# Optimization experiments

Measured on AMD Instinct MI355X. Metric: run time of the kernel, lower is better.

Reference implementation:

```python
import jax, jax.numpy as jnp
import numpy as np

D_MODEL = 1024
D_STATE = 64
D_CONV = 4
HEADDIM = 64
EXPAND = 2
NGROUPS = 1
D_INNER = EXPAND * D_MODEL            # 2048
NHEADS = D_INNER // HEADDIM           # 32
CONV_DIM = D_INNER + 2 * NGROUPS * D_STATE
D_IN_PROJ = 2 * D_INNER + 2 * NGROUPS * D_STATE + NHEADS
FFN_DIM = 4096
B_SZ = 2
SEQ = 2048


def layernorm(x, w, b, eps=1e-5):
    m = jnp.mean(x, axis=-1, keepdims=True)
    v = jnp.var(x, axis=-1, keepdims=True)
    return (x - m) * jax.lax.rsqrt(v + eps) * w + b


def silu(x):
    return x * jax.nn.sigmoid(x)


def causal_dwconv(x, w, b):
    # x: [B, L, C], w: [C, K] depthwise, b: [C]; causal (left) padding
    xc = jnp.transpose(x, (0, 2, 1))                       # [B, C, L]
    xc = jnp.pad(xc, ((0, 0), (0, 0), (D_CONV - 1, 0)))
    k = w[:, None, :]                                      # [C, 1, K]
    y = jax.lax.conv_general_dilated(
        xc, k, window_strides=(1,), padding='VALID',
        dimension_numbers=('NCH', 'OIH', 'NCH'),
        feature_group_count=CONV_DIM)
    return jnp.transpose(y, (0, 2, 1)) + b                 # [B, L, C]


def mamba2(x, in_proj_w, conv_w, conv_b, dt_bias, A_log, D_param, norm_w, out_proj_w):
    Bsz, L, _ = x.shape
    zxbcdt = x @ in_proj_w.T                               # [B, L, D_IN_PROJ]
    z, xBC, dt = jnp.split(zxbcdt, [D_INNER, D_INNER + CONV_DIM], axis=-1)
    dt = jax.nn.softplus(dt + dt_bias)                     # [B, L, H]
    xBC = silu(causal_dwconv(xBC, conv_w, conv_b))
    xs, Bm, Cm = jnp.split(xBC, [D_INNER, D_INNER + NGROUPS * D_STATE], axis=-1)
    xs = xs.reshape(Bsz, L, NHEADS, HEADDIM)
    Bm = Bm.reshape(Bsz, L, NGROUPS, D_STATE)
    Cm = Cm.reshape(Bsz, L, NGROUPS, D_STATE)
    hpg = NHEADS // NGROUPS
    Bh = jnp.repeat(Bm, hpg, axis=2)                       # [B, L, H, N]
    Ch = jnp.repeat(Cm, hpg, axis=2)                       # [B, L, H, N]
    A = -jnp.exp(A_log)                                    # [H]
    dA = jnp.exp(dt * A)                                   # [B, L, H]

    # time-major for scan
    def step(h, inp):
        dA_t, dt_t, x_t, B_t, C_t = inp                    # [B,H], [B,H], [B,H,P], [B,H,N], [B,H,N]
        h = h * dA_t[:, :, None, None] + (dt_t[:, :, None, None] * x_t[..., None]) * B_t[:, :, None, :]
        y_t = jnp.einsum('bhpn,bhn->bhp', h, C_t)
        return h, y_t

    h0 = jnp.zeros((Bsz, NHEADS, HEADDIM, D_STATE), dtype=x.dtype)
    xs_tm = (jnp.moveaxis(dA, 1, 0), jnp.moveaxis(dt, 1, 0),
             jnp.moveaxis(xs, 1, 0), jnp.moveaxis(Bh, 1, 0), jnp.moveaxis(Ch, 1, 0))
    _, ys = jax.lax.scan(step, h0, xs_tm)                  # [L, B, H, P]
    y = jnp.moveaxis(ys, 0, 1) + D_param[None, None, :, None] * xs
    y = y.reshape(Bsz, L, D_INNER)
    # gated RMSNorm: RMSNorm(y * silu(z)) * weight
    y = y * silu(z)
    y = y * jax.lax.rsqrt(jnp.mean(jnp.square(y), axis=-1, keepdims=True) + 1e-5) * norm_w
    return y @ out_proj_w.T                                # [B, L, D_MODEL]


def setup_inputs() -> dict:
    key = jax.random.key(0)
    ks = jax.random.split(key, 12)
    s = 0.02
    inp = {
        'x': jax.random.normal(ks[0], (B_SZ, SEQ, D_MODEL), dtype=jnp.float32),
        'ln0_w': jnp.ones((D_MODEL,), jnp.float32), 'ln0_b': jnp.zeros((D_MODEL,), jnp.float32),
        'ln1_w': jnp.ones((D_MODEL,), jnp.float32), 'ln1_b': jnp.zeros((D_MODEL,), jnp.float32),
        'ln2_w': jnp.ones((D_MODEL,), jnp.float32), 'ln2_b': jnp.zeros((D_MODEL,), jnp.float32),
        'in_proj_w': jax.random.normal(ks[1], (D_IN_PROJ, D_MODEL), jnp.float32) * s,
        'conv_w': jax.random.normal(ks[2], (CONV_DIM, D_CONV), jnp.float32) * 0.2,
        'conv_b': jnp.zeros((CONV_DIM,), jnp.float32),
        'dt_bias': jax.random.uniform(ks[3], (NHEADS,), jnp.float32, -4.0, -1.0),
        'A_log': jnp.log(jnp.arange(1, NHEADS + 1, dtype=jnp.float32)),
        'D_param': jnp.ones((NHEADS,), jnp.float32),
        'norm_w': jnp.ones((D_INNER,), jnp.float32),
        'out_proj_w': jax.random.normal(ks[4], (D_MODEL, D_INNER), jnp.float32) * s,
        'ffn_w1': jax.random.normal(ks[5], (FFN_DIM, D_MODEL), jnp.float32) * s,
        'ffn_b1': jnp.zeros((FFN_DIM,), jnp.float32),
        'ffn_w2': jax.random.normal(ks[6], (D_MODEL, FFN_DIM), jnp.float32) * s,
        'ffn_b2': jnp.zeros((D_MODEL,), jnp.float32),
    }
    return inp


def reference(x, ln0_w, ln0_b, ln1_w, ln1_b, ln2_w, ln2_b, in_proj_w, conv_w, conv_b,
              dt_bias, A_log, D_param, norm_w, out_proj_w, ffn_w1, ffn_b1, ffn_w2, ffn_b2):
    x = layernorm(x, ln0_w, ln0_b)                                  # ln0 (layer_id==0)
    m = mamba2(layernorm(x, ln1_w, ln1_b), in_proj_w, conv_w, conv_b,
               dt_bias, A_log, D_param, norm_w, out_proj_w)
    x = x + m                                                        # dropout is identity in eval
    h = layernorm(x, ln2_w, ln2_b)
    h = jax.nn.gelu(h @ ffn_w1.T + ffn_b1, approximate=False) @ ffn_w2.T + ffn_b2
    return x + h
```

## Files before the change

kernel.cpp:

```cpp
#include <hip/hip_runtime.h>
#include <hip/hip_bf16.h>
#include <math.h>

typedef __hip_bfloat16 bf16;
typedef __bf16 bhalf;
typedef bhalf bhalf8 __attribute__((ext_vector_type(8)));
typedef float f32x4 __attribute__((ext_vector_type(4)));
typedef unsigned short u16;
typedef u16 u16x4 __attribute__((ext_vector_type(4)));
typedef u16 u16x8 __attribute__((ext_vector_type(8)));

#define D_MODEL   1024
#define D_STATE   64
#define HEADDIM   64
#define D_INNER   2048
#define NHEADS    32
#define CONV_DIM  2176
#define D_IN_PROJ 4256
#define FFN_DIM   4096
#define BSZ       2
#define SEQ       2048
#define NROWS     (BSZ*SEQ)
#define TC        64
#define NCH       (SEQ/TC)

#define AS1 __attribute__((address_space(1)))
#define AS3 __attribute__((address_space(3)))
__device__ __forceinline__ void load_lds16(const void* g, void* l) {
  __builtin_amdgcn_global_load_lds((AS1 void*)g, (AS3 void*)l, 16, 0, 0);
}

__device__ __forceinline__ float bf2f(u16 u) {
  return __uint_as_float(((unsigned)u) << 16);
}
__device__ __forceinline__ u16 f2bbits(float f) {
  bf16 h = __float2bfloat16(f);
  return *(u16*)&h;
}

#define NT 18
struct CvtArgs {
  const void* src[NT];
  void*       dst[NT];
  int ccum[NT + 1];
  int nel[NT];
};

__global__ __launch_bounds__(256)
void cvt_kernel(CvtArgs a, const unsigned short* __restrict__ x0,
                int* __restrict__ flagp)
{
  __shared__ int sbad;
  if (threadIdx.x == 0) sbad = 0;
  __syncthreads();
  {
    float v = bf2f(x0[threadIdx.x]);
    if (!(fabsf(v) <= 1e6f)) sbad = 1;
  }
  __syncthreads();
  const int isf32 = sbad;
  if (blockIdx.x == 0 && threadIdx.x == 0) *flagp = isf32;

  int c = blockIdx.x;
  int ti = 0;
  while (c >= a.ccum[ti + 1]) ti++;
  int j = (c - a.ccum[ti]) * 2048 + threadIdx.x * 8;
  if (j >= a.nel[ti]) return;
  if (isf32) {
    const float* s = (const float*)a.src[ti];
    f32x4 v0 = *(const f32x4*)(s + j);
    f32x4 v1 = *(const f32x4*)(s + j + 4);
    u16x8 o;
    #pragma unroll
    for (int k = 0; k < 4; k++) { o[k] = f2bbits(v0[k]); o[k + 4] = f2bbits(v1[k]); }
    *(u16x8*)((u16*)a.dst[ti] + j) = o;
  } else {
    *(u16x8*)((u16*)a.dst[ti] + j) = *(const u16x8*)((const u16*)a.src[ti] + j);
  }
}

template<int EPI>
__global__ __launch_bounds__(256, 2)
void gemm_bt(const bf16* __restrict__ A, const bf16* __restrict__ W,
             int M, int N, int K,
             bf16* __restrict__ outB,
             const bf16* __restrict__ bias)
{
  __shared__ __align__(16) bhalf sA[2][128 * 64];
  __shared__ __align__(16) bhalf sW[2][128 * 64];
  const int n0   = blockIdx.x * 128;
  const int m0   = blockIdx.y * 128;
  const int t    = threadIdx.x;
  const int w    = t >> 6;
  const int lane = t & 63;
  const int wm   = (w >> 1) * 64;
  const int wn   = (w & 1) * 64;
  const int lr   = lane & 15;
  const int lq   = lane >> 4;

  f32x4 acc[4][4];
  #pragma unroll
  for (int i = 0; i < 4; i++)
    #pragma unroll
    for (int j = 0; j < 4; j++)
      acc[i][j] = (f32x4){0.f, 0.f, 0.f, 0.f};

  auto stage = [&](int buf, int kk0) {
    #pragma unroll
    for (int j = 0; j < 4; j++) {
      int s  = t + 256 * j;
      int r  = s >> 3;
      int cs = (s & 7) ^ (r & 7);
      load_lds16(A + (size_t)(m0 + r) * K + kk0 + cs * 8, &sA[buf][s * 8]);
      int wr = n0 + r; wr = wr < N ? wr : N - 1;
      load_lds16(W + (size_t)wr * K + kk0 + cs * 8, &sW[buf][s * 8]);
    }
  };

  stage(0, 0);
  __syncthreads();

  int cur = 0;
  for (int k0 = 0; k0 < K; k0 += 64) {
    if (k0 + 64 < K) stage(cur ^ 1, k0 + 64);
    const bhalf* pA = sA[cur];
    const bhalf* pW = sW[cur];
    #pragma unroll
    for (int kk = 0; kk < 2; kk++) {
      bhalf8 af[4], bfr[4];
      #pragma unroll
      for (int i = 0; i < 4; i++) {
        int r = wm + i * 16 + lr;
        int c = (kk * 4 + lq) ^ (r & 7);
        af[i] = *(const bhalf8*)(pA + r * 64 + c * 8);
      }
      #pragma unroll
      for (int j = 0; j < 4; j++) {
        int r = wn + j * 16 + lr;
        int c = (kk * 4 + lq) ^ (r & 7);
        bfr[j] = *(const bhalf8*)(pW + r * 64 + c * 8);
      }
      #pragma unroll
      for (int i = 0; i < 4; i++)
        #pragma unroll
        for (int j = 0; j < 4; j++)
          acc[i][j] = __builtin_amdgcn_mfma_f32_16x16x32_bf16(af[i], bfr[j], acc[i][j], 0, 0, 0);
    }
    __syncthreads();
    cur ^= 1;
  }

  #pragma unroll
  for (int i = 0; i < 4; i++) {
    #pragma unroll
    for (int j = 0; j < 4; j++) {
      #pragma unroll
      for (int r = 0; r < 4; r++) {
        int m = m0 + wm + i * 16 + lq * 4 + r;
        int n = n0 + wn + j * 16 + lr;
        if (n < N) {
          float v = acc[i][j][r];
          size_t idx = (size_t)m * N + n;
          if (EPI == 0) {
            outB[idx] = __float2bfloat16(v);
          } else {
            v += __bfloat162float(bias[n]);
            outB[idx] = __float2bfloat16(0.5f * v * (1.0f + erff(v * 0.70710678118654752f)));
          }
        }
      }
    }
  }
}

struct SkParts4 { float* p[4]; };

template<int SK>
__global__ __launch_bounds__(256, 4)
void gemm_skinny_sk(const bf16* __restrict__ A, const bf16* __restrict__ W,
                    int M, int N, int K, SkParts4 parts)
{
  __shared__ __align__(16) bhalf sA[64 * 64];
  __shared__ __align__(16) bhalf sW[128 * 64];
  const int id   = blockIdx.x;
  const int z    = id >> 9;
  const int id9  = id & 511;
  const int hi   = id9 >> 6;
  const int rem  = id9 & 63;
  const int jn   = rem >> 3;
  const int mi   = hi * 8 + (rem & 7);
  const int m0   = mi * 64;
  const int n0   = jn * 128;
  const int t    = threadIdx.x;
  const int w    = t >> 6;
  const int lane = t & 63;
  const int wm   = (w >> 1) * 32;
  const int wn   = (w & 1) * 64;
  const int lr   = lane & 15;
  const int lq   = lane >> 4;

  f32x4 acc[2][4];
  #pragma unroll
  for (int i = 0; i < 2; i++)
    #pragma unroll
    for (int j = 0; j < 4; j++)
      acc[i][j] = (f32x4){0.f, 0.f, 0.f, 0.f};

  const int kh = K / SK;
  const int kend = z * kh + kh;
  for (int k0 = z * kh; k0 < kend; k0 += 64) {
    #pragma unroll
    for (int j = 0; j < 2; j++) {
      int s  = t + 256 * j;
      int r  = s >> 3;
      int cs = (s & 7) ^ (r & 7);
      load_lds16(A + (size_t)(m0 + r) * K + k0 + cs * 8, sA + s * 8);
    }
    #pragma unroll
    for (int j = 0; j < 4; j++) {
      int s  = t + 256 * j;
      int r  = s >> 3;
      int cs = (s & 7) ^ (r & 7);
      load_lds16(W + (size_t)(n0 + r) * K + k0 + cs * 8, sW + s * 8);
    }
    __syncthreads();
    #pragma unroll
    for (int kk = 0; kk < 2; kk++) {
      bhalf8 af[2], bfr[4];
      #pragma unroll
      for (int i = 0; i < 2; i++) {
        int r = wm + i * 16 + lr;
        int c = (kk * 4 + lq) ^ (r & 7);
        af[i] = *(const bhalf8*)(sA + r * 64 + c * 8);
      }
      #pragma unroll
      for (int j = 0; j < 4; j++) {
        int r = wn + j * 16 + lr;
        int c = (kk * 4 + lq) ^ (r & 7);
        bfr[j] = *(const bhalf8*)(sW + r * 64 + c * 8);
      }
      #pragma unroll
      for (int i = 0; i < 2; i++)
        #pragma unroll
        for (int j = 0; j < 4; j++)
          acc[i][j] = __builtin_amdgcn_mfma_f32_16x16x32_bf16(af[i], bfr[j], acc[i][j], 0, 0, 0);
    }
    __syncthreads();
  }

  float* out = parts.p[z];
  #pragma unroll
  for (int i = 0; i < 2; i++)
    #pragma unroll
    for (int j = 0; j < 4; j++)
      #pragma unroll
      for (int r = 0; r < 4; r++) {
        int m = m0 + wm + i * 16 + lq * 4 + r;
        int n = n0 + wn + j * 16 + lr;
        out[(size_t)m * N + n] = acc[i][j][r];
      }
}

__global__ __launch_bounds__(256)
void reduce_out_ln2_kernel(const float* __restrict__ p0, const float* __restrict__ p1,
                           const bf16* __restrict__ resB, float* __restrict__ x2f,
                           const bf16* __restrict__ w, const bf16* __restrict__ b,
                           bf16* __restrict__ hln)
{
  int row = blockIdx.x, t = threadIdx.x;
  int i = row * 256 + t;
  __shared__ float rs[4], rq[4];
  f32x4 a = ((const f32x4*)p0)[i];
  f32x4 bb = ((const f32x4*)p1)[i];
  u16x4 r = ((const u16x4*)resB)[i];
  f32x4 o;
  float s = 0.f, ss = 0.f;
  #pragma unroll
  for (int j = 0; j < 4; j++) {
    o[j] = a[j] + bb[j] + bf2f(r[j]);
    s += o[j]; ss += o[j] * o[j];
  }
  ((f32x4*)x2f)[i] = o;
  #pragma unroll
  for (int off = 32; off; off >>= 1) { s += __shfl_down(s, off); ss += __shfl_down(ss, off); }
  if ((t & 63) == 0) { rs[t >> 6] = s; rq[t >> 6] = ss; }
  __syncthreads();
  float S = rs[0] + rs[1] + rs[2] + rs[3];
  float Q = rq[0] + rq[1] + rq[2] + rq[3];
  float mean = S * (1.f / D_MODEL);
  float rstd = rsqrtf(Q * (1.f / D_MODEL) - mean * mean + 1e-5f);
  u16x4 wv = ((const u16x4*)w)[t];
  u16x4 bv = ((const u16x4*)b)[t];
  u16x4 ov;
  #pragma unroll
  for (int j = 0; j < 4; j++)
    ov[j] = f2bbits((o[j] - mean) * rstd * bf2f(wv[j]) + bf2f(bv[j]));
  ((u16x4*)hln)[i] = ov;
}

__global__ __launch_bounds__(256)
void reduce_ffn_kernel(const float* __restrict__ p0, const float* __restrict__ p1,
                       const float* __restrict__ p2, const float* __restrict__ p3,
                       const bf16* __restrict__ bias, const float* __restrict__ resF,
                       void* __restrict__ outp, const int* __restrict__ flagp)
{
  int i = blockIdx.x * 256 + threadIdx.x;
  int n4 = i & (D_MODEL / 4 - 1);
  f32x4 v0 = ((const f32x4*)p0)[i];
  f32x4 v1 = ((const f32x4*)p1)[i];
  f32x4 v2 = ((const f32x4*)p2)[i];
  f32x4 v3 = ((const f32x4*)p3)[i];
  f32x4 rf = ((const f32x4*)resF)[i];
  u16x4 bb = ((const u16x4*)bias)[n4];
  f32x4 o;
  #pragma unroll
  for (int j = 0; j < 4; j++)
    o[j] = ((v0[j] + v1[j]) + (v2[j] + v3[j])) + rf[j] + bf2f(bb[j]);
  if (*flagp) {
    ((f32x4*)outp)[i] = o;
  } else {
    u16x4 ov;
    #pragma unroll
    for (int j = 0; j < 4; j++) ov[j] = f2bbits(o[j]);
    ((u16x4*)outp)[i] = ov;
  }
}

__global__ __launch_bounds__(256)
void ln01_kernel(const void* __restrict__ xin, const int* __restrict__ flagp,
                 const bf16* __restrict__ w0, const bf16* __restrict__ b0,
                 const bf16* __restrict__ w1, const bf16* __restrict__ b1,
                 bf16* __restrict__ x0o, bf16* __restrict__ x1o)
{
  int row = blockIdx.x, t = threadIdx.x;
  int i = row * 256 + t;
  __shared__ float rs[4], rq[4];
  float v[4], s = 0.f, ss = 0.f;
  if (*flagp) {
    f32x4 xv = ((const f32x4*)xin)[i];
    #pragma unroll
    for (int j = 0; j < 4; j++) v[j] = xv[j];
  } else {
    u16x4 xv = ((const u16x4*)xin)[i];
    #pragma unroll
    for (int j = 0; j < 4; j++) v[j] = bf2f(xv[j]);
  }
  #pragma unroll
  for (int j = 0; j < 4; j++) { s += v[j]; ss += v[j] * v[j]; }
  #pragma unroll
  for (int o = 32; o; o >>= 1) { s += __shfl_down(s, o); ss += __shfl_down(ss, o); }
  if ((t & 63) == 0) { rs[t >> 6] = s; rq[t >> 6] = ss; }
  __syncthreads();
  float S = rs[0] + rs[1] + rs[2] + rs[3];
  float Q = rq[0] + rq[1] + rq[2] + rq[3];
  float mean = S * (1.f / D_MODEL);
  float rstd = rsqrtf(Q * (1.f / D_MODEL) - mean * mean + 1e-5f);
  u16x4 w0v = ((const u16x4*)w0)[t], b0v = ((const u16x4*)b0)[t];
  float u[4]; s = 0.f; ss = 0.f;
  u16x4 o0;
  #pragma unroll
  for (int j = 0; j < 4; j++) {
    u[j] = (v[j] - mean) * rstd * bf2f(w0v[j]) + bf2f(b0v[j]);
    s += u[j]; ss += u[j] * u[j];
    o0[j] = f2bbits(u[j]);
  }
  ((u16x4*)x0o)[i] = o0;
  __syncthreads();
  #pragma unroll
  for (int o = 32; o; o >>= 1) { s += __shfl_down(s, o); ss += __shfl_down(ss, o); }
  if ((t & 63) == 0) { rs[t >> 6] = s; rq[t >> 6] = ss; }
  __syncthreads();
  S = rs[0] + rs[1] + rs[2] + rs[3];
  Q = rq[0] + rq[1] + rq[2] + rq[3];
  mean = S * (1.f / D_MODEL);
  rstd = rsqrtf(Q * (1.f / D_MODEL) - mean * mean + 1e-5f);
  u16x4 w1v = ((const u16x4*)w1)[t], b1v = ((const u16x4*)b1)[t];
  u16x4 o1;
  #pragma unroll
  for (int j = 0; j < 4; j++)
    o1[j] = f2bbits((u[j] - mean) * rstd * bf2f(w1v[j]) + bf2f(b1v[j]));
  ((u16x4*)x1o)[i] = o1;
}

__device__ __forceinline__ void conv8(const bf16* __restrict__ zxb,
                                      const bf16* __restrict__ cw,
                                      const bf16* __restrict__ cb,
                                      bf16* __restrict__ xact, int row, int c0)
{
  int l = row & (SEQ - 1);
  float acc[8];
  {
    bhalf8 cbv = *(const bhalf8*)(cb + c0);
    #pragma unroll
    for (int j = 0; j < 8; j++) acc[j] = (float)cbv[j];
  }
  bhalf wts[32];
  #pragma unroll
  for (int q = 0; q < 4; q++)
    *(bhalf8*)(wts + q * 8) = *(const bhalf8*)(cw + c0 * 4 + q * 8);
  #pragma unroll
  for (int k = 0; k < 4; k++) {
    int lt = l - 3 + k;
    if (lt >= 0) {
      bhalf8 xv = *(const bhalf8*)(zxb + (size_t)(row - 3 + k) * D_IN_PROJ + D_INNER + c0);
      #pragma unroll
      for (int j = 0; j < 8; j++)
        acc[j] = fmaf((float)xv[j], (float)wts[j * 4 + k], acc[j]);
    }
  }
  bhalf8 o;
  #pragma unroll
  for (int j = 0; j < 8; j++) {
    float a = acc[j];
    o[j] = (bhalf)(a / (1.f + expf(-a)));
  }
  *(bhalf8*)(xact + (size_t)row * CONV_DIM + c0) = o;
}

__global__ __launch_bounds__(256)
void conv_silu_dt_kernel(const bf16* __restrict__ zxb, const bf16* __restrict__ cw,
                         const bf16* __restrict__ cb, bf16* __restrict__ xact,
                         const bf16* __restrict__ dtb, const bf16* __restrict__ alog,
                         float* __restrict__ dts, float* __restrict__ ldab)
{
  const int row = blockIdx.y;
  const int t = threadIdx.x;
  if (blockIdx.x == 0) {
    conv8(zxb, cw, cb, xact, row, t * 8);
  } else {
    if (t < 16) {
      conv8(zxb, cw, cb, xact, row, 2048 + t * 8);
    } else if (t < 48) {
      int h = t - 16;
      float v = __bfloat162float(zxb[(size_t)row * D_IN_PROJ + (D_INNER + CONV_DIM) + h]) +
                __bfloat162float(dtb[h]);
      float sp = (v > 20.f) ? v : log1pf(expf(v));
      dts[row * NHEADS + h] = sp;
      ldab[row * NHEADS + h] = -sp * expf(__bfloat162float(alog[h]));
    }
  }
}

__global__ __launch_bounds__(256)
void scan_state_kernel(const bf16* __restrict__ xact, const float* __restrict__ dts,
                       const float* __restrict__ ldab, bf16* __restrict__ Sbuf,
                       float* __restrict__ acb)
{
  __shared__ __align__(16) bf16 wBT[64][72];
  __shared__ __align__(16) bf16 XT[64][72];
  __shared__ float lsS[64], dtS[64];
  const int bid = blockIdx.x;
  const int bh = bid & 63, c = bid >> 6;
  const int b = bh >> 5, h = bh & 31;
  const int t0 = c * TC;
  const int tid = threadIdx.x;
  const int w = tid >> 6, lane = tid & 63;
  const int lr = lane & 15, lq = lane >> 4;

  if (w == 0) {
    float v = ldab[(size_t)(b * SEQ + t0 + lane) * NHEADS + h];
    #pragma unroll
    for (int o = 1; o < 64; o <<= 1) {
      float up = __shfl_up(v, o);
      if (lane >= o) v += up;
    }
    lsS[lane] = v;
    dtS[lane] = dts[(size_t)(b * SEQ + t0 + lane) * NHEADS + h];
  }
  __syncthreads();
  const float lsT = lsS[63];
  {
    int nn = tid & 63, u0 = (tid >> 6) * 16;
    for (int i = 0; i < 16; i++) {
      int u = u0 + i;
      const bf16* rowp = xact + (size_t)(b * SEQ + t0 + u) * CONV_DIM;
      float wgt = dtS[u] * __expf(lsT - lsS[u]);
      wBT[nn][u] = __float2bfloat16(__bfloat162float(rowp[D_INNER + nn]) * wgt);
      XT[nn][u]  = rowp[h * 64 + nn];
    }
  }
  __syncthreads();

  bhalf8 af0 = *(const bhalf8*)&wBT[16 * w + lr][lq * 8];
  bhalf8 af1 = *(const bhalf8*)&wBT[16 * w + lr][32 + lq * 8];
  bf16* sb = Sbuf + ((size_t)bh * NCH + c) * 4096;
  #pragma unroll
  for (int jt = 0; jt < 4; jt++) {
    bhalf8 xf0 = *(const bhalf8*)&XT[16 * jt + lr][lq * 8];
    bhalf8 xf1 = *(const bhalf8*)&XT[16 * jt + lr][32 + lq * 8];
    f32x4 acc = (f32x4){0.f, 0.f, 0.f, 0.f};
    acc = __builtin_amdgcn_mfma_f32_16x16x32_bf16(af0, xf0, acc, 0, 0, 0);
    acc = __builtin_amdgcn_mfma_f32_16x16x32_bf16(af1, xf1, acc, 0, 0, 0);
    #pragma unroll
    for (int r = 0; r < 4; r++) {
      int n = 16 * w + lq * 4 + r;
      int p = 16 * jt + lr;
      sb[p * 64 + n] = __float2bfloat16(acc[r]);
    }
  }
  if (tid == 0) acb[bh * NCH + c] = __expf(lsT);
}

__global__ __launch_bounds__(256)
void state_prop_kernel(bf16* __restrict__ Sbuf, const float* __restrict__ acb)
{
  const int bh = blockIdx.x >> 2, q = blockIdx.x & 3;
  const int t = threadIdx.x;
  bf16* sp = Sbuf + (size_t)bh * NCH * 4096 + q * 1024 + t;
  const float* ap = acb + bh * NCH;
  float h0 = 0.f, h1 = 0.f, h2 = 0.f, h3 = 0.f;
  for (int c = 0; c < NCH; c++) {
    bf16* pc = sp + (size_t)c * 4096;
    float s0 = __bfloat162float(pc[0]);
    float s1 = __bfloat162float(pc[256]);
    float s2 = __bfloat162float(pc[512]);
    float s3 = __bfloat162float(pc[768]);
    float a = ap[c];
    pc[0]   = __float2bfloat16(h0);
    pc[256] = __float2bfloat16(h1);
    pc[512] = __float2bfloat16(h2);
    pc[768] = __float2bfloat16(h3);
    h0 = fmaf(h0, a, s0); h1 = fmaf(h1, a, s1);
    h2 = fmaf(h2, a, s2); h3 = fmaf(h3, a, s3);
  }
}

__global__ __launch_bounds__(256)
void scan_y_kernel(const bf16* __restrict__ xact, const float* __restrict__ dts,
                   const float* __restrict__ ldab, const bf16* __restrict__ Sbuf,
                   bf16* __restrict__ yfull)
{
  __shared__ __align__(16) bf16 Cs[64][72];
  __shared__ __align__(16) bf16 Bs[64][72];
  __shared__ __align__(16) bf16 XT[64][72];
  __shared__ __align__(16) bf16 HT[64][72];
  __shared__ float lsS[64], dtS[64];
  const int bid = blockIdx.x;
  const int bh = bid & 63, c = bid >> 6;
  const int b = bh >> 5, h = bh & 31;
  const int t0 = c * TC;
  const int tid = threadIdx.x;
  const int w = tid >> 6, lane = tid & 63;
  const int lr = lane & 15, lq = lane >> 4;

  if (w == 0) {
    float v = ldab[(size_t)(b * SEQ + t0 + lane) * NHEADS + h];
    #pragma unroll
    for (int o = 1; o < 64; o <<= 1) {
      float up = __shfl_up(v, o);
      if (lane >= o) v += up;
    }
    lsS[lane] = v;
    dtS[lane] = dts[(size_t)(b * SEQ + t0 + lane) * NHEADS + h];
  }
  {
    int nn = tid & 63, u0 = (tid >> 6) * 16;
    for (int i = 0; i < 16; i++) {
      int u = u0 + i;
      const bf16* rowp = xact + (size_t)(b * SEQ + t0 + u) * CONV_DIM;
      Bs[u][nn] = rowp[D_INNER + nn];
      Cs[u][nn] = rowp[D_INNER + 64 + nn];
      XT[nn][u] = rowp[h * 64 + nn];
    }
    const bf16* sb = Sbuf + ((size_t)bh * NCH + c) * 4096;
    for (int i = 0; i < 16; i++) {
      int e = tid + 256 * i;
      HT[e >> 6][e & 63] = sb[e];
    }
  }
  __syncthreads();

  bhalf8 cf0 = *(const bhalf8*)&Cs[16 * w + lr][lq * 8];
  bhalf8 cf1 = *(const bhalf8*)&Cs[16 * w + lr][32 + lq * 8];
  f32x4 accH[4];
  float mreg[4][4];
  #pragma unroll
  for (int jt = 0; jt < 4; jt++) {
    bhalf8 bf0 = *(const bhalf8*)&Bs[16 * jt + lr][lq * 8];
    bhalf8 bf1 = *(const bhalf8*)&Bs[16 * jt + lr][32 + lq * 8];
    f32x4 g = (f32x4){0.f, 0.f, 0.f, 0.f};
    g = __builtin_amdgcn_mfma_f32_16x16x32_bf16(cf0, bf0, g, 0, 0, 0);
    g = __builtin_amdgcn_mfma_f32_16x16x32_bf16(cf1, bf1, g, 0, 0, 0);
    bhalf8 hf0 = *(const bhalf8*)&HT[16 * jt + lr][lq * 8];
    bhalf8 hf1 = *(const bhalf8*)&HT[16 * jt + lr][32 + lq * 8];
    f32x4 ah = (f32x4){0.f, 0.f, 0.f, 0.f};
    ah = __builtin_amdgcn_mfma_f32_16x16x32_bf16(cf0, hf0, ah, 0, 0, 0);
    ah = __builtin_amdgcn_mfma_f32_16x16x32_bf16(cf1, hf1, ah, 0, 0, 0);
    accH[jt] = ah;
    #pragma unroll
    for (int r = 0; r < 4; r++) {
      int t = 16 * w + lq * 4 + r;
      int u = 16 * jt + lr;
      float m = 0.f;
      if (u <= t) m = g[r] * __expf(lsS[t] - lsS[u]) * dtS[u];
      mreg[jt][r] = m;
    }
  }
  __syncthreads();
  #pragma unroll
  for (int jt = 0; jt < 4; jt++)
    #pragma unroll
    for (int r = 0; r < 4; r++)
      Bs[16 * w + lq * 4 + r][16 * jt + lr] = __float2bfloat16(mreg[jt][r]);
  __syncthreads();

  bhalf8 mf0 = *(const bhalf8*)&Bs[16 * w + lr][lq * 8];
  bhalf8 mf1 = *(const bhalf8*)&Bs[16 * w + lr][32 + lq * 8];
  #pragma unroll
  for (int jt = 0; jt < 4; jt++) {
    bhalf8 xf0 = *(const bhalf8*)&XT[16 * jt + lr][lq * 8];
    bhalf8 xf1 = *(const bhalf8*)&XT[16 * jt + lr][32 + lq * 8];
    f32x4 acc = (f32x4){0.f, 0.f, 0.f, 0.f};
    acc = __builtin_amdgcn_mfma_f32_16x16x32_bf16(mf0, xf0, acc, 0, 0, 0);
    acc = __builtin_amdgcn_mfma_f32_16x16x32_bf16(mf1, xf1, acc, 0, 0, 0);
    #pragma unroll
    for (int r = 0; r < 4; r++) {
      int t = 16 * w + lq * 4 + r;
      int p = 16 * jt + lr;
      float y = acc[r] + __expf(lsS[t]) * accH[jt][r];
      yfull[(size_t)(b * SEQ + t0 + t) * D_INNER + h * 64 + p] = __float2bfloat16(y);
    }
  }
}

__global__ __launch_bounds__(256)
void gate_rms_kernel(const bf16* __restrict__ yfull, const bf16* __restrict__ xact,
                     const bf16* __restrict__ zxb, const bf16* __restrict__ Dp,
                     const bf16* __restrict__ nw, bf16* __restrict__ yn)
{
  int row = blockIdx.x, t = threadIdx.x;
  int c0 = t * 8;
  __shared__ float rq[4];
  bhalf8 yv8 = *(const bhalf8*)(yfull + (size_t)row * D_INNER + c0);
  bhalf8 xv8 = *(const bhalf8*)(xact + (size_t)row * CONV_DIM + c0);
  bhalf8 zv8 = *(const bhalf8*)(zxb + (size_t)row * D_IN_PROJ + c0);
  float Dv = __bfloat162float(Dp[c0 >> 6]);
  float yv[8]; float ss = 0.f;
  #pragma unroll
  for (int j = 0; j < 8; j++) {
    float y = (float)yv8[j] + Dv * (float)xv8[j];
    float z = (float)zv8[j];
    yv[j] = y * (z / (1.f + expf(-z)));
    ss += yv[j] * yv[j];
  }
  #pragma unroll
  for (int o = 32; o; o >>= 1) ss += __shfl_down(ss, o);
  if ((t & 63) == 0) rq[t >> 6] = ss;
  __syncthreads();
  float tot = rq[0] + rq[1] + rq[2] + rq[3];
  float rr = rsqrtf(tot * (1.f / D_INNER) + 1e-5f);
  bhalf8 nv8 = *(const bhalf8*)(nw + c0);
  bhalf8 o;
  #pragma unroll
  for (int j = 0; j < 8; j++)
    o[j] = (bhalf)(yv[j] * rr * (float)nv8[j]);
  *(bhalf8*)(yn + (size_t)row * D_INNER + c0) = o;
}

extern "C" void kernel_launch(void* const* d_in, const int* in_sizes, int n_in,
                              void* d_out, int out_size, void* d_ws, size_t ws_size,
                              hipStream_t stream)
{
  char* ws = (char*)d_ws;
  bf16*  x1b   = (bf16*) (ws + 0);
  bf16*  Sbuf  = (bf16*) (ws + 0);
  bf16*  ynb   = (bf16*) (ws + 0);
  float* pf0   = (float*)(ws + 0);
  bf16*  wproj = (bf16*) (ws + 16777216);
  float* acb   = (float*)(ws + 16777216);
  float* dtsb  = (float*)(ws + 16785408);
  float* ldab  = (float*)(ws + 17309696);
  float* pf1   = (float*)(ws + 16777216);
  bf16*  wout  = (bf16*) (ws + 25493504);
  bf16*  w1c   = (bf16*) (ws + 29687808);
  bf16*  w2c   = (bf16*) (ws + 38076416);
  bf16*  ln0w  = (bf16*) (ws + 46465024);
  bf16*  ln0b  = (bf16*) (ws + 46467072);
  bf16*  ln1w  = (bf16*) (ws + 46469120);
  bf16*  ln1b  = (bf16*) (ws + 46471168);
  bf16*  ln2w  = (bf16*) (ws + 46473216);
  bf16*  ln2b  = (bf16*) (ws + 46475264);
  bf16*  convw = (bf16*) (ws + 46477312);
  bf16*  convb = (bf16*) (ws + 46494720);
  bf16*  dtb   = (bf16*) (ws + 46499072);
  bf16*  alog  = (bf16*) (ws + 46499136);
  bf16*  Dp    = (bf16*) (ws + 46499200);
  bf16*  normw = (bf16*) (ws + 46499264);
  bf16*  b1c   = (bf16*) (ws + 46503360);
  bf16*  b2c   = (bf16*) (ws + 46511552);
  int*   flag  = (int*)  (ws + 46513600);
  bf16*  x0b   = (bf16*) (ws + 46514176);
  bf16*  zxb   = (bf16*) (ws + 54902784);
  float* x2f   = (float*)(ws + 54902784);
  float* pf3   = (float*)(ws + 71680000);
  bf16*  xact  = (bf16*) (ws + 89767936);
  float* pout0 = (float*)(ws + 89767936);
  float* pout1 = (float*)(ws + 106545152);
  bf16*  gbuf  = (bf16*) (ws + 89767936);
  bf16*  yfull = (bf16*) (ws + 125419520);
  bf16*  hln   = (bf16*) (ws + 125419520);
  float* pf2   = (float*)(ws + 125419520);

  CvtArgs ca;
  void* dsts[NT] = { ln0w, ln0b, ln1w, ln1b, ln2w, ln2b, wproj, convw, convb,
                     dtb, alog, Dp, normw, wout, w1c, b1c, w2c, b2c };
  int cc = 0;
  ca.ccum[0] = 0;
  for (int i = 0; i < NT; i++) {
    ca.src[i] = d_in[i + 1];
    ca.dst[i] = dsts[i];
    ca.nel[i] = in_sizes[i + 1];
    cc += (in_sizes[i + 1] + 2047) / 2048;
    ca.ccum[i + 1] = cc;
  }
  cvt_kernel<<<cc, 256, 0, stream>>>(ca, (const unsigned short*)d_in[0], flag);

  ln01_kernel<<<NROWS, 256, 0, stream>>>(d_in[0], flag, ln0w, ln0b, ln1w, ln1b,
                                         x0b, x1b);

  gemm_bt<0><<<dim3(34, 32), 256, 0, stream>>>(x1b, wproj, NROWS, D_IN_PROJ, D_MODEL,
                                               zxb, nullptr);

  conv_silu_dt_kernel<<<dim3(2, NROWS), 256, 0, stream>>>(zxb, convw, convb, xact,
                                                          dtb, alog, dtsb, ldab);

  scan_state_kernel<<<NCH * 64, 256, 0, stream>>>(xact, dtsb, ldab, Sbuf, acb);
  state_prop_kernel<<<64 * 4, 256, 0, stream>>>(Sbuf, acb);
  scan_y_kernel<<<NCH * 64, 256, 0, stream>>>(xact, dtsb, ldab, Sbuf, yfull);

  gate_rms_kernel<<<NROWS, 256, 0, stream>>>(yfull, xact, zxb, Dp, normw, ynb);

  SkParts4 po = { { pout0, pout1, pout0, pout0 } };
  gemm_skinny_sk<2><<<1024, 256, 0, stream>>>(ynb, wout, NROWS, D_MODEL, D_INNER, po);
  reduce_out_ln2_kernel<<<NROWS, 256, 0, stream>>>(pout0, pout1, x0b, x2f,
                                                   ln2w, ln2b, hln);

  gemm_bt<2><<<dim3(32, 32), 256, 0, stream>>>(hln, w1c, NROWS, FFN_DIM, D_MODEL,
                                               gbuf, b1c);

  SkParts4 pfp = { { pf0, pf1, pf2, pf3 } };
  gemm_skinny_sk<4><<<2048, 256, 0, stream>>>(gbuf, w2c, NROWS, D_MODEL, FFN_DIM, pfp);
  reduce_ffn_kernel<<<(NROWS * D_MODEL) / 1024, 256, 0, stream>>>(pf0, pf1, pf2, pf3,
                                                                  b2c, x2f, d_out, flag);
}
```

Baseline: 442.9 us.

## Use 256x256-tile double-buffered GEMM kernel for FFN up-projection

Adds a new GEMM kernel with 256x256 output tiles, 512 threads (8 waves each computing 128x64), and double-buffered LDS staging with async loads, and uses it for the FFN first projection with the GELU epilogue. Larger tiles raise arithmetic intensity and cut global/LDS reload traffic compared to the previous 128x128 kernel. It uses 128KB of LDS and many accumulator registers, and the grid shrinks to 256 blocks, which may underfill the GPU's CUs or lower occupancy.

Result: no change. 449.0 us (+1.4%).

```diff
diff --git a/kernel.cpp b/kernel.cpp
--- a/kernel.cpp
+++ b/kernel.cpp
@@ -167,6 +167,109 @@
             v += __bfloat162float(bias[n]);
             outB[idx] = __float2bfloat16(0.5f * v * (1.0f + erff(v * 0.70710678118654752f)));
           }
+        }
+      }
+    }
+  }
+}
+
+template<int EPI>
+__global__ __launch_bounds__(512, 2)
+void gemm256_bt(const bf16* __restrict__ A, const bf16* __restrict__ W,
+                int M, int N, int K,
+                bf16* __restrict__ outB,
+                const bf16* __restrict__ bias)
+{
+  __shared__ __align__(16) bhalf sA[2][256 * 64];
+  __shared__ __align__(16) bhalf sW[2][256 * 64];
+  const int n0   = blockIdx.x * 256;
+  const int m0   = blockIdx.y * 256;
+  const int t    = threadIdx.x;
+  const int w    = t >> 6;
+  const int lane = t & 63;
+  const int wm   = (w >> 2) * 128;
+  const int wn   = (w & 3) * 64;
+  const int lr   = lane & 15;
+  const int lq   = lane >> 4;
+
+  f32x4 acc[8][4];
+  #pragma unroll
+  for (int i = 0; i < 8; i++)
+    #pragma unroll
+    for (int j = 0; j < 4; j++)
+      acc[i][j] = (f32x4){0.f, 0.f, 0.f, 0.f};
+
+  auto stage = [&](int buf, int kk0) {
+    #pragma unroll
+    for (int j = 0; j < 4; j++) {
+      int s  = t + 512 * j;
+      int r  = s >> 3;
+      int cs = (s & 7) ^ (r & 7);
+      load_lds16(A + (size_t)(m0 + r) * K + kk0 + cs * 8, &sA[buf][s * 8]);
+    }
+    #pragma unroll
+    for (int j = 0; j < 4; j++) {
+      int s  = t + 512 * j;
+      int r  = s >> 3;
+      int cs = (s & 7) ^ (r & 7);
+      load_lds16(W + (size_t)(n0 + r) * K + kk0 + cs * 8, &sW[buf][s * 8]);
+    }
+  };
+
+  stage(0, 0);
+
+  int cur = 0;
+  for (int k0 = 0; k0 < K; k0 += 64) {
+    const bool more = (k0 + 64 < K);
+    if (more) stage(cur ^ 1, k0 + 64);
+    if (more) asm volatile("s_waitcnt vmcnt(8)" ::: "memory");
+    else      asm volatile("s_waitcnt vmcnt(0)" ::: "memory");
+    __builtin_amdgcn_s_barrier();
+    asm volatile("" ::: "memory");
+
+    const bhalf* pA = sA[cur];
+    const bhalf* pW = sW[cur];
+    #pragma unroll
+    for (int kk = 0; kk < 2; kk++) {
+      bhalf8 af[8], bfr[4];
+      #pragma unroll
+      for (int i = 0; i < 8; i++) {
+        int r = wm + i * 16 + lr;
+        int c = (kk * 4 + lq) ^ (r & 7);
+        af[i] = *(const bhalf8*)(pA + r * 64 + c * 8);
+      }
+      #pragma unroll
+      for (int j = 0; j < 4; j++) {
+        int r = wn + j * 16 + lr;
+        int c = (kk * 4 + lq) ^ (r & 7);
+        bfr[j] = *(const bhalf8*)(pW + r * 64 + c * 8);
+      }
+      #pragma unroll
+      for (int i = 0; i < 8; i++)
+        #pragma unroll
+        for (int j = 0; j < 4; j++)
+          acc[i][j] = __builtin_amdgcn_mfma_f32_16x16x32_bf16(af[i], bfr[j], acc[i][j], 0, 0, 0);
+    }
+    __builtin_amdgcn_s_barrier();
+    asm volatile("" ::: "memory");
+    cur ^= 1;
+  }
+
+  #pragma unroll
+  for (int i = 0; i < 8; i++) {
+    #pragma unroll
+    for (int j = 0; j < 4; j++) {
+      #pragma unroll
+      for (int r = 0; r < 4; r++) {
+        int m = m0 + wm + i * 16 + lq * 4 + r;
+        int n = n0 + wn + j * 16 + lr;
+        float v = acc[i][j][r];
+        size_t idx = (size_t)m * N + n;
+        if (EPI == 0) {
+          outB[idx] = __float2bfloat16(v);
+        } else {
+          v += __bfloat162float(bias[n]);
+          outB[idx] = __float2bfloat16(0.5f * v * (1.0f + erff(v * 0.70710678118654752f)));
         }
       }
     }
@@ -735,8 +838,8 @@
   reduce_out_ln2_kernel<<<NROWS, 256, 0, stream>>>(pout0, pout1, x0b, x2f,
                                                    ln2w, ln2b, hln);
 
-  gemm_bt<2><<<dim3(32, 32), 256, 0, stream>>>(hln, w1c, NROWS, FFN_DIM, D_MODEL,
-                                               gbuf, b1c);
+  gemm256_bt<2><<<dim3(16, 16), 512, 0, stream>>>(hln, w1c, NROWS, FFN_DIM, D_MODEL,
+                                                  gbuf, b1c);
 
   SkParts4 pfp = { { pf0, pf1, pf2, pf3 } };
   gemm_skinny_sk<4><<<2048, 256, 0, stream>>>(gbuf, w2c, NROWS, D_MODEL, FFN_DIM, pfp);
```
